# Performance work log

Hardware: AMD Instinct MI355X
Metric: run time of the kernel (lower is better)

Reference implementation:

```python
import jax, jax.numpy as jnp
import numpy as np
import math

N_HEADS = 16
THETA = 10000.0


def setup_inputs() -> dict:
    key = jax.random.key(0)
    ks = jax.random.split(key, 5)
    B, T, D = 4, 2048, 1024
    return {
        "x": jax.random.normal(ks[0], (B, T, D), dtype=jnp.float32),
        "w_qkv": jax.random.normal(ks[1], (3 * D, D), dtype=jnp.float32) * 0.02,
        "b_qkv": jax.random.normal(ks[2], (3 * D,), dtype=jnp.float32) * 0.02,
        "w_out": jax.random.normal(ks[3], (D, D), dtype=jnp.float32) * 0.02,
        "b_out": jax.random.normal(ks[4], (D,), dtype=jnp.float32) * 0.02,
    }


def reference(x, w_qkv, b_qkv, w_out, b_out):
    B, T, D = x.shape
    H = N_HEADS
    hd = D // H
    half = hd // 2

    # fused QKV projection (nn.Linear: y = x @ W^T + b)
    qkv = (x @ w_qkv.T + b_qkv).reshape(B, T, 3, H, hd)
    q, k, v = qkv[:, :, 0], qkv[:, :, 1], qkv[:, :, 2]

    # RoPE: interleaved (even, odd) pairs treated as complex, rotated by e^{i t w}
    inv_freq = 1.0 / (THETA ** (jnp.arange(0, hd, 2, dtype=jnp.float32) / hd))  # [half]
    angles = jnp.arange(T, dtype=jnp.float32)[:, None] * inv_freq[None, :]      # [T, half]
    cos = jnp.cos(angles)[None, :, None, :]  # [1,T,1,half]
    sin = jnp.sin(angles)[None, :, None, :]

    def rotate(t):
        tr = t.reshape(B, T, H, half, 2)
        te, to = tr[..., 0], tr[..., 1]
        rot = jnp.stack([te * cos - to * sin, te * sin + to * cos], axis=-1)
        return rot.reshape(B, T, H, hd).astype(t.dtype)

    q, k = rotate(q), rotate(k)

    # non-causal SDPA, scale = 1/sqrt(head_dim)
    scale = 1.0 / math.sqrt(hd)
    scores = jnp.einsum("bqhd,bkhd->bhqk", q, k) * scale
    attn = jax.nn.softmax(scores, axis=-1)
    out = jnp.einsum("bhqk,bkhd->bqhd", attn, v).reshape(B, T, D)

    return out @ w_out.T + b_out
```

## Files before the change

kernel.cpp:

```cpp
#include <hip/hip_runtime.h>

typedef __attribute__((ext_vector_type(4))) float f32x4;
typedef __attribute__((ext_vector_type(16))) float f32x16;
typedef __attribute__((ext_vector_type(8))) short bf16x8;
typedef __attribute__((ext_vector_type(4))) unsigned u32x4;

__device__ __forceinline__ unsigned short f2bf(float f) {
  unsigned u = __float_as_uint(f);
  u += 0x7fff + ((u >> 16) & 1);
  return (unsigned short)(u >> 16);
}
__device__ __forceinline__ float bf2f(unsigned short h) {
  return __uint_as_float(((unsigned)h) << 16);
}

__device__ __forceinline__ void gload_lds16(const void* g, void* lds) {
  __builtin_amdgcn_global_load_lds(
      (const __attribute__((address_space(1))) unsigned int*)g,
      (__attribute__((address_space(3))) unsigned int*)lds, 16, 0, 0);
}

__global__ void cast_f32_bf16(const float* __restrict__ in,
                              unsigned short* __restrict__ out, int n4) {
  int i = blockIdx.x * blockDim.x + threadIdx.x;
  if (i >= n4) return;
  float4 v = ((const float4*)in)[i];
  ushort4 o;
  o.x = f2bf(v.x); o.y = f2bf(v.y); o.z = f2bf(v.z); o.w = f2bf(v.w);
  ((ushort4*)out)[i] = o;
}

__global__ void rope_table(float2* __restrict__ cs) {
  int idx = blockIdx.x * blockDim.x + threadIdx.x;
  if (idx >= 2048 * 32) return;
  int t = idx >> 5, i = idx & 31;
  float inv = powf(10000.0f, -(float)(2 * i) / 64.0f);
  float a = (float)t * inv;
  cs[idx] = make_float2(cosf(a), sinf(a));
}

__global__ void rope_apply(unsigned short* __restrict__ qkv,
                           const float2* __restrict__ cs) {
  int idx = blockIdx.x * blockDim.x + threadIdx.x;
  int i = idx & 31;
  int h = (idx >> 5) & 15;
  int t = (idx >> 9) & 2047;
  int b = idx >> 20;
  float2 v = cs[(t << 5) | i];
  size_t base = ((size_t)((b << 11) + t)) * 3072 + h * 64 + 2 * i;
#pragma unroll
  for (int part = 0; part < 2; ++part) {
    unsigned short* p = qkv + base + part * 1024;
    unsigned pr = *(unsigned*)p;
    float e = bf2f((unsigned short)(pr & 0xffff));
    float o = bf2f((unsigned short)(pr >> 16));
    float ne = e * v.x - o * v.y;
    float no = e * v.y + o * v.x;
    *(unsigned*)p = (unsigned)f2bf(ne) | ((unsigned)f2bf(no) << 16);
  }
}

template <int OUT_BF16>
__global__ __launch_bounds__(256, 2) void gemm_bt(
    const unsigned short* __restrict__ A, const unsigned short* __restrict__ B,
    const float* __restrict__ bias, void* __restrict__ Cout,
    int M, int N, int K) {
  __shared__ unsigned short lA[128 * 64];
  __shared__ unsigned short lB[128 * 64];
  const int tiles_n = N >> 7;
  const int bm = blockIdx.x / tiles_n;
  const int bn = blockIdx.x % tiles_n;
  const int tid = threadIdx.x;
  const int w = tid >> 6, l = tid & 63;
  const int l15 = l & 15, lq = l >> 4;
  const int wm = (w >> 1) * 64, wn = (w & 1) * 64;
  const int m0 = bm << 7, n0 = bn << 7;
  const int arow = l >> 3;
  const int acol = (l & 7) * 8;
  f32x4 acc[4][4] = {};

  for (int k0 = 0; k0 < K; k0 += 64) {
    __syncthreads();
#pragma unroll
    for (int it = 0; it < 4; ++it) {
      const int rb = it * 32 + w * 8;
      gload_lds16(A + (size_t)(m0 + rb + arow) * K + k0 + acol, &lA[rb * 64]);
      gload_lds16(B + (size_t)(n0 + rb + arow) * K + k0 + acol, &lB[rb * 64]);
    }
    __syncthreads();
#pragma unroll
    for (int ks = 0; ks < 2; ++ks) {
      bf16x8 af[4], bfr[4];
#pragma unroll
      for (int mi = 0; mi < 4; ++mi)
        af[mi] = *(const bf16x8*)&lA[(wm + mi * 16 + l15) * 64 + ks * 32 + lq * 8];
#pragma unroll
      for (int ni = 0; ni < 4; ++ni)
        bfr[ni] = *(const bf16x8*)&lB[(wn + ni * 16 + l15) * 64 + ks * 32 + lq * 8];
#pragma unroll
      for (int mi = 0; mi < 4; ++mi)
#pragma unroll
        for (int ni = 0; ni < 4; ++ni)
          acc[mi][ni] = __builtin_amdgcn_mfma_f32_16x16x32_bf16(
              af[mi], bfr[ni], acc[mi][ni], 0, 0, 0);
    }
  }

#pragma unroll
  for (int ni = 0; ni < 4; ++ni) {
    const int c = n0 + wn + ni * 16 + l15;
    const float bv = bias[c];
#pragma unroll
    for (int mi = 0; mi < 4; ++mi) {
#pragma unroll
      for (int j = 0; j < 4; ++j) {
        const int r = m0 + wm + mi * 16 + lq * 4 + j;
        const float v = acc[mi][ni][j] + bv;
        if (OUT_BF16)
          ((unsigned short*)Cout)[(size_t)r * N + c] = f2bf(v);
        else
          ((float*)Cout)[(size_t)r * N + c] = v;
      }
    }
  }
}

__global__ __launch_bounds__(256, 3) void attn_fwd(
    const unsigned short* __restrict__ qkv, unsigned short* __restrict__ aout) {
  __shared__ unsigned short lK[2 * 64 * 64];
  __shared__ unsigned short lVt[2 * 64 * 72];

  const int g = blockIdx.x;
  const int xcd = g & 7;
  const int j2 = g >> 3;
  const int bh = ((j2 >> 4) << 3) + xcd;
  const int qt = j2 & 15;
  const int h = bh & 15, b = bh >> 4;

  const int tid = threadIdx.x;
  const int w = tid >> 6, l = tid & 63;
  const int l31 = l & 31, hi = l >> 5;
  const int l7 = l & 7;

  const size_t bt_base = (size_t)(b * 2048) * 3072;
  const int qbase = qt * 128 + w * 32;

  const unsigned short* Qp =
      qkv + bt_base + (size_t)(qbase + l31) * 3072 + h * 64 + hi * 8;
  bf16x8 qf[4];
#pragma unroll
  for (int s = 0; s < 4; ++s) {
    bf16x8 q = *(const bf16x8*)(Qp + 16 * s);
#pragma unroll
    for (int e = 0; e < 8; ++e)
      q[e] = (short)f2bf(bf2f((unsigned short)q[e]) * 0.125f);
    qf[s] = q;
  }

  const unsigned short* Kp = qkv + bt_base + 1024 + h * 64;
  const unsigned short* Vp = qkv + bt_base + 2048 + h * 64;

  const int krow = l >> 3;
  const int kcol = ((l & 7) ^ (l >> 3)) << 3;

  const int vr = tid >> 2;
  const int vc0 = (tid & 3) << 4;

  f32x16 o0 = {}, o1 = {};
  float m_run = -1e30f, lsum = 0.f;
  bf16x8 v0, v1;
  const float L2E = 1.4426950408889634f;

  {
    gload_lds16(Kp + (size_t)(w * 8 + krow) * 3072 + kcol, &lK[(w * 8) * 64]);
    gload_lds16(Kp + (size_t)(32 + w * 8 + krow) * 3072 + kcol, &lK[(32 + w * 8) * 64]);
    const unsigned short* vb = Vp + (size_t)vr * 3072 + vc0;
    v0 = *(const bf16x8*)vb;
    v1 = *(const bf16x8*)(vb + 8);
#pragma unroll
    for (int i2 = 0; i2 < 8; ++i2) {
      lVt[(vc0 + i2) * 72 + (vr ^ vc0)] = (unsigned short)v0[i2];
      lVt[(vc0 + 8 + i2) * 72 + (vr ^ vc0)] = (unsigned short)v1[i2];
    }
  }
  __syncthreads();

  for (int kt = 0; kt < 32; ++kt) {
    const int cur = kt & 1;
    const unsigned short* lKc = lK + cur * 4096;
    const unsigned short* lVc = lVt + cur * 4608;
    const bool stage = (kt < 31);

    if (stage) {
      const unsigned short* kb = Kp + (size_t)(kt + 1) * 64 * 3072;
      unsigned short* lKn = lK + (cur ^ 1) * 4096;
      gload_lds16(kb + (size_t)(w * 8 + krow) * 3072 + kcol, lKn + (w * 8) * 64);
      gload_lds16(kb + (size_t)(32 + w * 8 + krow) * 3072 + kcol, lKn + (32 + w * 8) * 64);
      const unsigned short* vb = Vp + (size_t)(kt + 1) * 64 * 3072 + (size_t)vr * 3072 + vc0;
      v0 = *(const bf16x8*)vb;
      v1 = *(const bf16x8*)(vb + 8);
    }

    f32x16 sa[2] = {{}, {}};
    __builtin_amdgcn_s_setprio(1);
#pragma unroll
    for (int kt2 = 0; kt2 < 2; ++kt2) {
#pragma unroll
      for (int s = 0; s < 4; ++s) {
        bf16x8 kf = *(const bf16x8*)&lKc[(kt2 * 32 + l31) * 64 + (((2 * s + hi) ^ l7) << 3)];
        sa[kt2] = __builtin_amdgcn_mfma_f32_32x32x16_bf16(kf, qf[s], sa[kt2], 0, 0, 0);
      }
    }
    __builtin_amdgcn_s_setprio(0);

    float pmax = -1e30f;
#pragma unroll
    for (int r = 0; r < 16; r += 2) {
      float t0, t1;
      asm("v_max3_f32 %0, %1, %2, %3"
          : "=v"(t0) : "v"(sa[0][r]), "v"(sa[0][r + 1]), "v"(pmax));
      asm("v_max3_f32 %0, %1, %2, %3"
          : "=v"(t1) : "v"(sa[1][r]), "v"(sa[1][r + 1]), "v"(t0));
      pmax = t1;
    }
    pmax = fmaxf(pmax, __shfl_xor(pmax, 32));
    if (!__all(pmax <= m_run + 8.0f)) {
      const float mn = fmaxf(m_run, pmax);
      const float alpha = __expf(m_run - mn);
      m_run = mn;
      lsum *= alpha;
#pragma unroll
      for (int r = 0; r < 16; ++r) {
        const float ar = __shfl(alpha, (r & 3) + 8 * (r >> 2) + 4 * hi);
        o0[r] *= ar;
        o1[r] *= ar;
      }
    }
    const float m2 = m_run * L2E;
    float rsa = 0.f, rsb = 0.f;
#pragma unroll
    for (int kt2 = 0; kt2 < 2; ++kt2) {
#pragma unroll
      for (int r = 0; r < 16; r += 2) {
        const float a0 = __builtin_fmaf(sa[kt2][r], L2E, -m2);
        const float a1 = __builtin_fmaf(sa[kt2][r + 1], L2E, -m2);
        float p0, p1;
        asm("v_exp_f32 %0, %1" : "=v"(p0) : "v"(a0));
        asm("v_exp_f32 %0, %1" : "=v"(p1) : "v"(a1));
        sa[kt2][r] = p0;
        sa[kt2][r + 1] = p1;
        rsa += p0;
        rsb += p1;
      }
    }
    float rs = rsa + rsb;
    rs += __shfl_xor(rs, 32);
    lsum += rs;

    __builtin_amdgcn_s_setprio(1);
#pragma unroll
    for (int ks = 0; ks < 4; ++ks) {
      const int kt2 = ks >> 1, k2 = (ks & 1) * 8;
      unsigned xa, xb, ya, yb;
      asm("v_cvt_pk_bf16_f32 %0, %1, %2"
          : "=v"(xa) : "v"(sa[kt2][k2 + 0]), "v"(sa[kt2][k2 + 1]));
      asm("v_cvt_pk_bf16_f32 %0, %1, %2"
          : "=v"(xb) : "v"(sa[kt2][k2 + 2]), "v"(sa[kt2][k2 + 3]));
      asm("v_cvt_pk_bf16_f32 %0, %1, %2"
          : "=v"(ya) : "v"(sa[kt2][k2 + 4]), "v"(sa[kt2][k2 + 5]));
      asm("v_cvt_pk_bf16_f32 %0, %1, %2"
          : "=v"(yb) : "v"(sa[kt2][k2 + 6]), "v"(sa[kt2][k2 + 7]));
      asm("v_permlane32_swap_b32 %0, %1" : "+v"(xa), "+v"(ya));
      asm("v_permlane32_swap_b32 %0, %1" : "+v"(xb), "+v"(yb));
      u32x4 pw;
      pw[0] = xa; pw[1] = xb; pw[2] = ya; pw[3] = yb;
      const bf16x8 pa = __builtin_bit_cast(bf16x8, pw);
#pragma unroll
      for (int nd = 0; nd < 2; ++nd) {
        const int vrow = nd * 32 + l31;
        const bf16x8 vf = *(const bf16x8*)
            &lVc[vrow * 72 + ((16 * ks + 8 * hi) ^ (vrow & 0x30))];
        if (nd == 0)
          o0 = __builtin_amdgcn_mfma_f32_32x32x16_bf16(pa, vf, o0, 0, 0, 0);
        else
          o1 = __builtin_amdgcn_mfma_f32_32x32x16_bf16(pa, vf, o1, 0, 0, 0);
      }
    }
    __builtin_amdgcn_s_setprio(0);

    if (stage) {
      unsigned short* lVn = lVt + (cur ^ 1) * 4608;
#pragma unroll
      for (int i2 = 0; i2 < 8; ++i2) {
        lVn[(vc0 + i2) * 72 + (vr ^ vc0)] = (unsigned short)v0[i2];
        lVn[(vc0 + 8 + i2) * 72 + (vr ^ vc0)] = (unsigned short)v1[i2];
      }
    }
    __syncthreads();
  }

  const float linv = 1.0f / lsum;
#pragma unroll
  for (int r = 0; r < 16; ++r) {
    const int crow = (r & 3) + 8 * (r >> 2) + 4 * hi;
    const float lr = __shfl(linv, crow);
    unsigned short* orow =
        aout + (size_t)(b * 2048 + qbase + crow) * 1024 + h * 64 + l31;
    orow[0] = f2bf(o0[r] * lr);
    orow[32] = f2bf(o1[r] * lr);
  }
}

extern "C" void kernel_launch(void* const* d_in, const int* in_sizes, int n_in,
                              void* d_out, int out_size, void* d_ws, size_t ws_size,
                              hipStream_t stream) {
  const float* x     = (const float*)d_in[0];
  const float* w_qkv = (const float*)d_in[1];
  const float* b_qkv = (const float*)d_in[2];
  const float* w_out = (const float*)d_in[3];
  const float* b_out = (const float*)d_in[4];
  float* out = (float*)d_out;

  char* ws = (char*)d_ws;
  unsigned short* x_bf    = (unsigned short*)(ws);
  unsigned short* wqkv_bf = (unsigned short*)(ws + 16777216);
  unsigned short* wout_bf = (unsigned short*)(ws + 23068672);
  unsigned short* qkv     = (unsigned short*)(ws + 25165824);
  unsigned short* aout    = (unsigned short*)(ws + 75497472);
  float2* cs              = (float2*)(ws + 92274688);

  cast_f32_bf16<<<2097152 / 256, 256, 0, stream>>>(x, x_bf, 2097152);
  cast_f32_bf16<<<786432 / 256, 256, 0, stream>>>(w_qkv, wqkv_bf, 786432);
  cast_f32_bf16<<<262144 / 256, 256, 0, stream>>>(w_out, wout_bf, 262144);
  rope_table<<<65536 / 256, 256, 0, stream>>>(cs);

  gemm_bt<1><<<64 * 24, 256, 0, stream>>>(x_bf, wqkv_bf, b_qkv, qkv,
                                          8192, 3072, 1024);
  rope_apply<<<4194304 / 256, 256, 0, stream>>>(qkv, cs);
  attn_fwd<<<1024, 256, 0, stream>>>(qkv, aout);
  gemm_bt<0><<<64 * 8, 256, 0, stream>>>(aout, wout_bf, b_out, out,
                                         8192, 1024, 1024);
}
```

Before: 230.0 us.

## Software-pipeline QK^T one tile ahead and fuse Q RoPE into attention

The attention loop is restructured so the QK^T MFMAs for the next key tile are issued while softmax and PV of the current tile run, using two alternating score register sets. K prefetch moves two tiles ahead and the V global load is delayed until after the V LDS write. RoPE on Q is folded into the attention kernel's Q load, so the standalone rope kernel only touches K and moves half the memory traffic. The extra score registers raise VGPR pressure and may reduce occupancy or cause spills.

```diff
diff --git a/kernel.cpp b/kernel.cpp
--- a/kernel.cpp
+++ b/kernel.cpp
@@ -39,25 +39,22 @@
   cs[idx] = make_float2(cosf(a), sinf(a));
 }
 
-__global__ void rope_apply(unsigned short* __restrict__ qkv,
-                           const float2* __restrict__ cs) {
+__global__ void rope_apply_k(unsigned short* __restrict__ qkv,
+                             const float2* __restrict__ cs) {
   int idx = blockIdx.x * blockDim.x + threadIdx.x;
   int i = idx & 31;
   int h = (idx >> 5) & 15;
   int t = (idx >> 9) & 2047;
   int b = idx >> 20;
   float2 v = cs[(t << 5) | i];
-  size_t base = ((size_t)((b << 11) + t)) * 3072 + h * 64 + 2 * i;
-#pragma unroll
-  for (int part = 0; part < 2; ++part) {
-    unsigned short* p = qkv + base + part * 1024;
-    unsigned pr = *(unsigned*)p;
-    float e = bf2f((unsigned short)(pr & 0xffff));
-    float o = bf2f((unsigned short)(pr >> 16));
-    float ne = e * v.x - o * v.y;
-    float no = e * v.y + o * v.x;
-    *(unsigned*)p = (unsigned)f2bf(ne) | ((unsigned)f2bf(no) << 16);
-  }
+  unsigned short* p =
+      qkv + ((size_t)((b << 11) + t)) * 3072 + 1024 + h * 64 + 2 * i;
+  unsigned pr = *(unsigned*)p;
+  float e = bf2f((unsigned short)(pr & 0xffff));
+  float o = bf2f((unsigned short)(pr >> 16));
+  float ne = e * v.x - o * v.y;
+  float no = e * v.y + o * v.x;
+  *(unsigned*)p = (unsigned)f2bf(ne) | ((unsigned)f2bf(no) << 16);
 }
 
 template <int OUT_BF16>
@@ -126,7 +123,8 @@
 }
 
 __global__ __launch_bounds__(256, 3) void attn_fwd(
-    const unsigned short* __restrict__ qkv, unsigned short* __restrict__ aout) {
+    const unsigned short* __restrict__ qkv, unsigned short* __restrict__ aout,
+    const float2* __restrict__ cs) {
   __shared__ unsigned short lK[2 * 64 * 64];
   __shared__ unsigned short lVt[2 * 64 * 72];
 
@@ -147,13 +145,19 @@
 
   const unsigned short* Qp =
       qkv + bt_base + (size_t)(qbase + l31) * 3072 + h * 64 + hi * 8;
+  const float2* csrow = cs + (size_t)(qbase + l31) * 32;
   bf16x8 qf[4];
 #pragma unroll
   for (int s = 0; s < 4; ++s) {
     bf16x8 q = *(const bf16x8*)(Qp + 16 * s);
 #pragma unroll
-    for (int e = 0; e < 8; ++e)
-      q[e] = (short)f2bf(bf2f((unsigned short)q[e]) * 0.125f);
+    for (int j = 0; j < 4; ++j) {
+      const float2 cn = csrow[8 * s + 4 * hi + j];
+      const float e = bf2f((unsigned short)q[2 * j]);
+      const float o = bf2f((unsigned short)q[2 * j + 1]);
+      q[2 * j]     = (short)f2bf((e * cn.x - o * cn.y) * 0.125f);
+      q[2 * j + 1] = (short)f2bf((e * cn.y + o * cn.x) * 0.125f);
+    }
     qf[s] = q;
   }
 
@@ -170,6 +174,8 @@
   float m_run = -1e30f, lsum = 0.f;
   bf16x8 v0, v1;
   const float L2E = 1.4426950408889634f;
+
+  f32x16 saA[2], saB[2];
 
   {
     gload_lds16(Kp + (size_t)(w * 8 + krow) * 3072 + kcol, &lK[(w * 8) * 64]);
@@ -177,50 +183,66 @@
     const unsigned short* vb = Vp + (size_t)vr * 3072 + vc0;
     v0 = *(const bf16x8*)vb;
     v1 = *(const bf16x8*)(vb + 8);
+  }
+  __syncthreads();
+  {
+    saA[0] = (f32x16){};
+    saA[1] = (f32x16){};
+#pragma unroll
+    for (int kt2 = 0; kt2 < 2; ++kt2)
+#pragma unroll
+      for (int s = 0; s < 4; ++s) {
+        bf16x8 kf = *(const bf16x8*)&lK[(kt2 * 32 + l31) * 64 + (((2 * s + hi) ^ l7) << 3)];
+        saA[kt2] = __builtin_amdgcn_mfma_f32_32x32x16_bf16(kf, qf[s], saA[kt2], 0, 0, 0);
+      }
 #pragma unroll
     for (int i2 = 0; i2 < 8; ++i2) {
       lVt[(vc0 + i2) * 72 + (vr ^ vc0)] = (unsigned short)v0[i2];
       lVt[(vc0 + 8 + i2) * 72 + (vr ^ vc0)] = (unsigned short)v1[i2];
     }
+    const unsigned short* kb = Kp + (size_t)64 * 3072;
+    gload_lds16(kb + (size_t)(w * 8 + krow) * 3072 + kcol, &lK[4096 + (w * 8) * 64]);
+    gload_lds16(kb + (size_t)(32 + w * 8 + krow) * 3072 + kcol, &lK[4096 + (32 + w * 8) * 64]);
+    const unsigned short* vb = Vp + (size_t)64 * 3072 + (size_t)vr * 3072 + vc0;
+    v0 = *(const bf16x8*)vb;
+    v1 = *(const bf16x8*)(vb + 8);
   }
   __syncthreads();
 
-  for (int kt = 0; kt < 32; ++kt) {
-    const int cur = kt & 1;
-    const unsigned short* lKc = lK + cur * 4096;
+  auto body = [&](int t, f32x16* sc, f32x16* sn) {
+    const int cur = t & 1;
     const unsigned short* lVc = lVt + cur * 4608;
-    const bool stage = (kt < 31);
-
-    if (stage) {
-      const unsigned short* kb = Kp + (size_t)(kt + 1) * 64 * 3072;
-      unsigned short* lKn = lK + (cur ^ 1) * 4096;
+
+    if (t < 30) {
+      const unsigned short* kb = Kp + (size_t)(t + 2) * 64 * 3072;
+      unsigned short* lKn = lK + cur * 4096;
       gload_lds16(kb + (size_t)(w * 8 + krow) * 3072 + kcol, lKn + (w * 8) * 64);
       gload_lds16(kb + (size_t)(32 + w * 8 + krow) * 3072 + kcol, lKn + (32 + w * 8) * 64);
-      const unsigned short* vb = Vp + (size_t)(kt + 1) * 64 * 3072 + (size_t)vr * 3072 + vc0;
-      v0 = *(const bf16x8*)vb;
-      v1 = *(const bf16x8*)(vb + 8);
-    }
-
-    f32x16 sa[2] = {{}, {}};
-    __builtin_amdgcn_s_setprio(1);
-#pragma unroll
-    for (int kt2 = 0; kt2 < 2; ++kt2) {
-#pragma unroll
-      for (int s = 0; s < 4; ++s) {
-        bf16x8 kf = *(const bf16x8*)&lKc[(kt2 * 32 + l31) * 64 + (((2 * s + hi) ^ l7) << 3)];
-        sa[kt2] = __builtin_amdgcn_mfma_f32_32x32x16_bf16(kf, qf[s], sa[kt2], 0, 0, 0);
-      }
-    }
-    __builtin_amdgcn_s_setprio(0);
+    }
+
+    if (t < 31) {
+      const unsigned short* lKn = lK + (cur ^ 1) * 4096;
+      sn[0] = (f32x16){};
+      sn[1] = (f32x16){};
+      __builtin_amdgcn_s_setprio(1);
+#pragma unroll
+      for (int kt2 = 0; kt2 < 2; ++kt2)
+#pragma unroll
+        for (int s = 0; s < 4; ++s) {
+          bf16x8 kf = *(const bf16x8*)&lKn[(kt2 * 32 + l31) * 64 + (((2 * s + hi) ^ l7) << 3)];
+          sn[kt2] = __builtin_amdgcn_mfma_f32_32x32x16_bf16(kf, qf[s], sn[kt2], 0, 0, 0);
+        }
+      __builtin_amdgcn_s_setprio(0);
+    }
 
     float pmax = -1e30f;
 #pragma unroll
     for (int r = 0; r < 16; r += 2) {
       float t0, t1;
       asm("v_max3_f32 %0, %1, %2, %3"
-          : "=v"(t0) : "v"(sa[0][r]), "v"(sa[0][r + 1]), "v"(pmax));
+          : "=v"(t0) : "v"(sc[0][r]), "v"(sc[0][r + 1]), "v"(pmax));
       asm("v_max3_f32 %0, %1, %2, %3"
-          : "=v"(t1) : "v"(sa[1][r]), "v"(sa[1][r + 1]), "v"(t0));
+          : "=v"(t1) : "v"(sc[1][r]), "v"(sc[1][r + 1]), "v"(t0));
       pmax = t1;
     }
     pmax = fmaxf(pmax, __shfl_xor(pmax, 32));
@@ -242,13 +264,13 @@
     for (int kt2 = 0; kt2 < 2; ++kt2) {
 #pragma unroll
       for (int r = 0; r < 16; r += 2) {
-        const float a0 = __builtin_fmaf(sa[kt2][r], L2E, -m2);
-        const float a1 = __builtin_fmaf(sa[kt2][r + 1], L2E, -m2);
+        const float a0 = __builtin_fmaf(sc[kt2][r], L2E, -m2);
+        const float a1 = __builtin_fmaf(sc[kt2][r + 1], L2E, -m2);
         float p0, p1;
         asm("v_exp_f32 %0, %1" : "=v"(p0) : "v"(a0));
         asm("v_exp_f32 %0, %1" : "=v"(p1) : "v"(a1));
-        sa[kt2][r] = p0;
-        sa[kt2][r + 1] = p1;
+        sc[kt2][r] = p0;
+        sc[kt2][r + 1] = p1;
         rsa += p0;
         rsb += p1;
       }
@@ -263,13 +285,13 @@
       const int kt2 = ks >> 1, k2 = (ks & 1) * 8;
       unsigned xa, xb, ya, yb;
       asm("v_cvt_pk_bf16_f32 %0, %1, %2"
-          : "=v"(xa) : "v"(sa[kt2][k2 + 0]), "v"(sa[kt2][k2 + 1]));
+          : "=v"(xa) : "v"(sc[kt2][k2 + 0]), "v"(sc[kt2][k2 + 1]));
       asm("v_cvt_pk_bf16_f32 %0, %1, %2"
-          : "=v"(xb) : "v"(sa[kt2][k2 + 2]), "v"(sa[kt2][k2 + 3]));
+          : "=v"(xb) : "v"(sc[kt2][k2 + 2]), "v"(sc[kt2][k2 + 3]));
       asm("v_cvt_pk_bf16_f32 %0, %1, %2"
-          : "=v"(ya) : "v"(sa[kt2][k2 + 4]), "v"(sa[kt2][k2 + 5]));
+          : "=v"(ya) : "v"(sc[kt2][k2 + 4]), "v"(sc[kt2][k2 + 5]));
       asm("v_cvt_pk_bf16_f32 %0, %1, %2"
-          : "=v"(yb) : "v"(sa[kt2][k2 + 6]), "v"(sa[kt2][k2 + 7]));
+          : "=v"(yb) : "v"(sc[kt2][k2 + 6]), "v"(sc[kt2][k2 + 7]));
       asm("v_permlane32_swap_b32 %0, %1" : "+v"(xa), "+v"(ya));
       asm("v_permlane32_swap_b32 %0, %1" : "+v"(xb), "+v"(yb));
       u32x4 pw;
@@ -288,7 +310,7 @@
     }
     __builtin_amdgcn_s_setprio(0);
 
-    if (stage) {
+    if (t < 31) {
       unsigned short* lVn = lVt + (cur ^ 1) * 4608;
 #pragma unroll
       for (int i2 = 0; i2 < 8; ++i2) {
@@ -296,7 +318,18 @@
         lVn[(vc0 + 8 + i2) * 72 + (vr ^ vc0)] = (unsigned short)v1[i2];
       }
     }
+    if (t < 30) {
+      const unsigned short* vb =
+          Vp + (size_t)(t + 2) * 64 * 3072 + (size_t)vr * 3072 + vc0;
+      v0 = *(const bf16x8*)vb;
+      v1 = *(const bf16x8*)(vb + 8);
+    }
     __syncthreads();
+  };
+
+  for (int t = 0; t < 32; t += 2) {
+    body(t, saA, saB);
+    body(t + 1, saB, saA);
   }
 
   const float linv = 1.0f / lsum;
@@ -336,8 +369,8 @@
 
   gemm_bt<1><<<64 * 24, 256, 0, stream>>>(x_bf, wqkv_bf, b_qkv, qkv,
                                           8192, 3072, 1024);
-  rope_apply<<<4194304 / 256, 256, 0, stream>>>(qkv, cs);
-  attn_fwd<<<1024, 256, 0, stream>>>(qkv, aout);
+  rope_apply_k<<<4194304 / 256, 256, 0, stream>>>(qkv, cs);
+  attn_fwd<<<1024, 256, 0, stream>>>(qkv, aout, cs);
   gemm_bt<0><<<64 * 8, 256, 0, stream>>>(aout, wout_bf, b_out, out,
                                          8192, 1024, 1024);
 }
```

After: 254.0 us. 1.1x slower.
